# Kernel optimization log

Measured on AMD Instinct MI355X. Metric: run time of the kernel, lower is better.

Reference implementation:

```python
import jax, jax.numpy as jnp
import numpy as np

NUM_CLASSES = 10
LAMBDA_COORD = 5.0
LAMBDA_NOOBJ = 0.5
B, S, P = 2048, 26, 5 + NUM_CLASSES


def setup_inputs() -> dict:
    key = jax.random.key(0)
    k1, k2 = jax.random.split(key)
    predictions = jax.random.normal(k1, (B, S, S, P), dtype=jnp.float32)
    targets = jax.random.normal(k2, (B, S * S * P,), dtype=jnp.float32)
    return {"predictions": predictions, "targets": targets}


def reference(predictions, targets):
    b, s, _, p = predictions.shape
    pred = predictions.reshape(b, s * s, p)          # (B, S*S, 5+C)
    tgt = targets.reshape(b, s * s, -1)              # (B, S*S, 5+C)

    obj = tgt[..., 4] > 0                            # object mask per cell

    # Coordinate loss: lambda_coord * sum((pred_xywh - tgt_xywh)^2) over object cells
    coord_sq = jnp.sum((pred[..., :4] - tgt[..., :4]) ** 2, axis=-1)
    coord_loss = LAMBDA_COORD * jnp.sum(jnp.where(obj, coord_sq, 0.0))

    # Confidence loss: (sigmoid(p_conf) - t_conf)^2 on obj cells,
    # lambda_noobj * sigmoid(p_conf)^2 on no-obj cells (scalar MSE mean == squared diff)
    conf_p = jax.nn.sigmoid(pred[..., 4])
    conf_loss = jnp.sum(jnp.where(obj,
                                  (conf_p - tgt[..., 4]) ** 2,
                                  LAMBDA_NOOBJ * conf_p ** 2))

    # Classification loss: mean over C of squared diff per object cell, summed
    cls_sq = jnp.mean((pred[..., 5:5 + NUM_CLASSES] - tgt[..., 5:5 + NUM_CLASSES]) ** 2, axis=-1)
    class_loss = jnp.sum(jnp.where(obj, cls_sq, 0.0))

    total_loss = coord_loss + conf_loss + class_loss
    return (total_loss, coord_loss, conf_loss, class_loss)
```

## Files before the change

kernel.cpp:

```cpp
#include <hip/hip_runtime.h>

constexpr int   NUM_CLASSES  = 10;
constexpr float LAMBDA_COORD = 5.0f;
constexpr float LAMBDA_NOOBJ = 0.5f;
constexpr int   BLOCK = 256;
constexpr int   CELLS_PER_TILE = 256;
constexpr int   F4_PER_TILE    = 960;
constexpr int   NBLOCKS_MAX    = 2048;

__global__ __launch_bounds__(BLOCK) void yolo_main(
    const float4* __restrict__ pred4,
    const float4* __restrict__ tgt4,
    float* __restrict__ ws,
    unsigned ntiles, unsigned nblocks)
{
    __shared__ float flag[CELLS_PER_TILE + 1];

    const unsigned tid  = threadIdx.x;
    const bool     has3 = tid < (unsigned)(F4_PER_TILE - 768);

    float coord = 0.f, conf = 0.f, cls = 0.f;

    for (unsigned tile = blockIdx.x; tile < ntiles; tile += nblocks) {
        const unsigned tb = tile * F4_PER_TILE;

        float4 t[4], p[4];
        t[0] = tgt4[tb + tid];
        t[1] = tgt4[tb + tid + 256u];
        t[2] = tgt4[tb + tid + 512u];
        t[3] = has3 ? tgt4[tb + tid + 768u] : float4{0.f, 0.f, 0.f, 0.f};
        p[0] = pred4[tb + tid];
        p[1] = pred4[tb + tid + 256u];
        p[2] = pred4[tb + tid + 512u];
        p[3] = has3 ? pred4[tb + tid + 768u] : float4{0.f, 0.f, 0.f, 0.f};

        __syncthreads();

#pragma unroll
        for (int q = 0; q < 4; ++q) {
            if (q == 3 && !has3) continue;
            unsigned lb    = 4u * (tid + 256u * (unsigned)q);
            unsigned lcell = lb / 15u;
            unsigned j0    = lb - lcell * 15u;
            float tm[4] = {t[q].x, t[q].y, t[q].z, t[q].w};
#pragma unroll
            for (int m = 0; m < 4; ++m) {
                unsigned j   = j0 + (unsigned)m;
                bool     sec = j >= 15u;
                unsigned jj  = sec ? j - 15u : j;
                if (jj == 4u) flag[lcell + (sec ? 1u : 0u)] = tm[m];
            }
        }
        __syncthreads();

#pragma unroll
        for (int q = 0; q < 4; ++q) {
            if (q == 3 && !has3) continue;
            unsigned lb    = 4u * (tid + 256u * (unsigned)q);
            unsigned lcell = lb / 15u;
            unsigned j0    = lb - lcell * 15u;
            float t4a = flag[lcell];
            float t4b = flag[lcell + 1u];
            float pm[4] = {p[q].x, p[q].y, p[q].z, p[q].w};
            float tm[4] = {t[q].x, t[q].y, t[q].z, t[q].w};

            float pc = 0.f, tc = 0.f;
            bool  hasc = false;

#pragma unroll
            for (int m = 0; m < 4; ++m) {
                unsigned j   = j0 + (unsigned)m;
                bool     sec = j >= 15u;
                unsigned jj  = sec ? j - 15u : j;
                float    t4  = sec ? t4b : t4a;
                bool     obj = t4 > 0.f;

                float d  = pm[m] - tm[m];
                float sq = d * d;

                if (jj == 4u) { pc = pm[m]; tc = tm[m]; hasc = true; }
                else if (obj) {
                    if (jj < 4u) coord += sq;
                    else         cls   += sq;
                }
            }
            if (hasc) {
                float e   = __expf(-pc);
                float sig = __builtin_amdgcn_rcpf(1.f + e);
                float ds  = sig - tc;
                conf += (tc > 0.f) ? ds * ds : LAMBDA_NOOBJ * sig * sig;
            }
        }
    }

#pragma unroll
    for (int off = 32; off > 0; off >>= 1) {
        coord += __shfl_down(coord, off);
        conf  += __shfl_down(conf,  off);
        cls   += __shfl_down(cls,   off);
    }

    __shared__ float s[3][4];
    int wave = threadIdx.x >> 6, lane = threadIdx.x & 63;
    if (lane == 0) { s[0][wave] = coord; s[1][wave] = conf; s[2][wave] = cls; }
    __syncthreads();

    if (threadIdx.x == 0) {
        ws[blockIdx.x]               = s[0][0] + s[0][1] + s[0][2] + s[0][3];
        ws[nblocks + blockIdx.x]     = s[1][0] + s[1][1] + s[1][2] + s[1][3];
        ws[2 * nblocks + blockIdx.x] = s[2][0] + s[2][1] + s[2][2] + s[2][3];
    }
}

__global__ __launch_bounds__(BLOCK) void yolo_finalize(
    const float* __restrict__ ws, float* __restrict__ out, unsigned nblocks)
{
    float c0 = 0.f, c1 = 0.f, c2 = 0.f;
    for (unsigned i = threadIdx.x; i < nblocks; i += BLOCK) {
        c0 += ws[i];
        c1 += ws[nblocks + i];
        c2 += ws[2 * nblocks + i];
    }
#pragma unroll
    for (int off = 32; off > 0; off >>= 1) {
        c0 += __shfl_down(c0, off);
        c1 += __shfl_down(c1, off);
        c2 += __shfl_down(c2, off);
    }
    __shared__ float s[3][4];
    int wave = threadIdx.x >> 6, lane = threadIdx.x & 63;
    if (lane == 0) { s[0][wave] = c0; s[1][wave] = c1; s[2][wave] = c2; }
    __syncthreads();
    if (threadIdx.x == 0) {
        float coord = LAMBDA_COORD * (s[0][0] + s[0][1] + s[0][2] + s[0][3]);
        float conf  =                 s[1][0] + s[1][1] + s[1][2] + s[1][3];
        float cls   = (1.f / NUM_CLASSES) * (s[2][0] + s[2][1] + s[2][2] + s[2][3]);
        out[0] = coord + conf + cls;
        out[1] = coord;
        out[2] = conf;
        out[3] = cls;
    }
}

extern "C" void kernel_launch(void* const* d_in, const int* in_sizes, int n_in,
                              void* d_out, int out_size, void* d_ws, size_t ws_size,
                              hipStream_t stream) {
    const float* pred = (const float*)d_in[0];
    const float* tgt  = (const float*)d_in[1];
    float* out = (float*)d_out;
    float* ws  = (float*)d_ws;

    unsigned total  = (unsigned)in_sizes[0];
    unsigned ncells = total / 15u;
    unsigned ntiles = ncells / CELLS_PER_TILE;

    unsigned nblocks = NBLOCKS_MAX;
    if ((size_t)nblocks * 3 * sizeof(float) > ws_size)
        nblocks = (unsigned)(ws_size / (3 * sizeof(float)));
    if (nblocks > ntiles) nblocks = ntiles;

    yolo_main<<<nblocks, BLOCK, 0, stream>>>(
        (const float4*)pred, (const float4*)tgt, ws, ntiles, nblocks);
    yolo_finalize<<<1, BLOCK, 0, stream>>>(ws, out, nblocks);
}
```

Baseline: 184.8 us.

## Use per-wave tiles with one-shot blocks and binned atomic partial sums

Replaces the grid-stride loop over 256-cell block tiles with a one-shot grid in which each wave handles its own 64-cell tile, using a per-wave LDS flag array. This removes the block-wide barriers between the flag-write and compute phases. Per-block partials are now atomically added into 256 bins zeroed by a memset, so finalize reads a fixed number of entries. The cost is a much larger grid, an extra memset launch, atomic contention on the bins, and a change in the order of float summation.

Result: no change. 183.5 us (-0.7%).

```diff
diff --git a/kernel.cpp b/kernel.cpp
--- a/kernel.cpp
+++ b/kernel.cpp
@@ -4,92 +4,90 @@
 constexpr float LAMBDA_COORD = 5.0f;
 constexpr float LAMBDA_NOOBJ = 0.5f;
 constexpr int   BLOCK = 256;
-constexpr int   CELLS_PER_TILE = 256;
-constexpr int   F4_PER_TILE    = 960;
-constexpr int   NBLOCKS_MAX    = 2048;
+constexpr int   CELLS_PER_WAVE = 64;
+constexpr int   F4_PER_WAVE    = 240;
+constexpr int   NBINS = 256;
 
 __global__ __launch_bounds__(BLOCK) void yolo_main(
     const float4* __restrict__ pred4,
     const float4* __restrict__ tgt4,
-    float* __restrict__ ws,
-    unsigned ntiles, unsigned nblocks)
+    float* __restrict__ ws)
 {
-    __shared__ float flag[CELLS_PER_TILE + 1];
+    __shared__ float flag[4][CELLS_PER_WAVE + 1];
 
     const unsigned tid  = threadIdx.x;
-    const bool     has3 = tid < (unsigned)(F4_PER_TILE - 768);
+    const unsigned wave = tid >> 6;
+    const unsigned lane = tid & 63u;
+    const bool     has3 = lane < 48u;
+
+    const unsigned gw = blockIdx.x * 4u + wave;
+    const unsigned fb = gw * F4_PER_WAVE;
+
+    float4 t[4], p[4];
+    t[0] = tgt4[fb + lane];
+    t[1] = tgt4[fb + 64u + lane];
+    t[2] = tgt4[fb + 128u + lane];
+    t[3] = has3 ? tgt4[fb + 192u + lane] : float4{0.f, 0.f, 0.f, 0.f};
+    p[0] = pred4[fb + lane];
+    p[1] = pred4[fb + 64u + lane];
+    p[2] = pred4[fb + 128u + lane];
+    p[3] = has3 ? pred4[fb + 192u + lane] : float4{0.f, 0.f, 0.f, 0.f};
+
+#pragma unroll
+    for (int q = 0; q < 4; ++q) {
+        unsigned lf4 = (q < 3) ? (lane + 64u * (unsigned)q) : (192u + lane);
+        unsigned lb  = 4u * lf4;
+        unsigned lcell = lb / 15u;
+        unsigned j0    = lb - lcell * 15u;
+        float tm[4] = {t[q].x, t[q].y, t[q].z, t[q].w};
+#pragma unroll
+        for (int m = 0; m < 4; ++m) {
+            if (q == 3 && !has3) break;
+            unsigned j   = j0 + (unsigned)m;
+            bool     sec = j >= 15u;
+            unsigned jj  = sec ? j - 15u : j;
+            if (jj == 4u) flag[wave][lcell + (sec ? 1u : 0u)] = tm[m];
+        }
+    }
 
     float coord = 0.f, conf = 0.f, cls = 0.f;
+#pragma unroll
+    for (int q = 0; q < 4; ++q) {
+        unsigned lf4 = (q < 3) ? (lane + 64u * (unsigned)q) : (192u + lane);
+        unsigned lb  = 4u * lf4;
+        unsigned lcell = lb / 15u;
+        unsigned j0    = lb - lcell * 15u;
+        float t4a = flag[wave][lcell];
+        float t4b = flag[wave][lcell + 1u];
+        float pm[4] = {p[q].x, p[q].y, p[q].z, p[q].w};
+        float tm[4] = {t[q].x, t[q].y, t[q].z, t[q].w};
 
-    for (unsigned tile = blockIdx.x; tile < ntiles; tile += nblocks) {
-        const unsigned tb = tile * F4_PER_TILE;
-
-        float4 t[4], p[4];
-        t[0] = tgt4[tb + tid];
-        t[1] = tgt4[tb + tid + 256u];
-        t[2] = tgt4[tb + tid + 512u];
-        t[3] = has3 ? tgt4[tb + tid + 768u] : float4{0.f, 0.f, 0.f, 0.f};
-        p[0] = pred4[tb + tid];
-        p[1] = pred4[tb + tid + 256u];
-        p[2] = pred4[tb + tid + 512u];
-        p[3] = has3 ? pred4[tb + tid + 768u] : float4{0.f, 0.f, 0.f, 0.f};
-
-        __syncthreads();
+        float pc = 0.f, tc = 0.f;
+        bool  hasc = false;
 
 #pragma unroll
-        for (int q = 0; q < 4; ++q) {
-            if (q == 3 && !has3) continue;
-            unsigned lb    = 4u * (tid + 256u * (unsigned)q);
-            unsigned lcell = lb / 15u;
-            unsigned j0    = lb - lcell * 15u;
-            float tm[4] = {t[q].x, t[q].y, t[q].z, t[q].w};
-#pragma unroll
-            for (int m = 0; m < 4; ++m) {
-                unsigned j   = j0 + (unsigned)m;
-                bool     sec = j >= 15u;
-                unsigned jj  = sec ? j - 15u : j;
-                if (jj == 4u) flag[lcell + (sec ? 1u : 0u)] = tm[m];
+        for (int m = 0; m < 4; ++m) {
+            if (q == 3 && !has3) break;
+            unsigned j   = j0 + (unsigned)m;
+            bool     sec = j >= 15u;
+            unsigned jj  = sec ? j - 15u : j;
+            float    t4  = sec ? t4b : t4a;
+            bool     obj = t4 > 0.f;
+
+            float d  = pm[m] - tm[m];
+            float sq = d * d;
+
+            if (jj == 4u) { pc = pm[m]; tc = tm[m]; hasc = true; }
+            else if (obj) {
+                if (jj < 4u) coord += sq;
+                else         cls   += sq;
             }
         }
-        __syncthreads();
-
-#pragma unroll
-        for (int q = 0; q < 4; ++q) {
-            if (q == 3 && !has3) continue;
-            unsigned lb    = 4u * (tid + 256u * (unsigned)q);
-            unsigned lcell = lb / 15u;
-            unsigned j0    = lb - lcell * 15u;
-            float t4a = flag[lcell];
-            float t4b = flag[lcell + 1u];
-            float pm[4] = {p[q].x, p[q].y, p[q].z, p[q].w};
-            float tm[4] = {t[q].x, t[q].y, t[q].z, t[q].w};
-
-            float pc = 0.f, tc = 0.f;
-            bool  hasc = false;
-
-#pragma unroll
-            for (int m = 0; m < 4; ++m) {
-                unsigned j   = j0 + (unsigned)m;
-                bool     sec = j >= 15u;
-                unsigned jj  = sec ? j - 15u : j;
-                float    t4  = sec ? t4b : t4a;
-                bool     obj = t4 > 0.f;
-
-                float d  = pm[m] - tm[m];
-                float sq = d * d;
-
-                if (jj == 4u) { pc = pm[m]; tc = tm[m]; hasc = true; }
-                else if (obj) {
-                    if (jj < 4u) coord += sq;
-                    else         cls   += sq;
-                }
-            }
-            if (hasc) {
-                float e   = __expf(-pc);
-                float sig = __builtin_amdgcn_rcpf(1.f + e);
-                float ds  = sig - tc;
-                conf += (tc > 0.f) ? ds * ds : LAMBDA_NOOBJ * sig * sig;
-            }
+        if (hasc) {
+            float e   = __expf(-pc);
+            float sig = __builtin_amdgcn_rcpf(1.f + e);
+            float ds  = sig - tc;
+            conf += (tc > 0.f) ? ds * ds : LAMBDA_NOOBJ * sig * sig;
         }
     }
 
@@ -101,25 +99,25 @@
     }
 
     __shared__ float s[3][4];
-    int wave = threadIdx.x >> 6, lane = threadIdx.x & 63;
     if (lane == 0) { s[0][wave] = coord; s[1][wave] = conf; s[2][wave] = cls; }
     __syncthreads();
 
-    if (threadIdx.x == 0) {
-        ws[blockIdx.x]               = s[0][0] + s[0][1] + s[0][2] + s[0][3];
-        ws[nblocks + blockIdx.x]     = s[1][0] + s[1][1] + s[1][2] + s[1][3];
-        ws[2 * nblocks + blockIdx.x] = s[2][0] + s[2][1] + s[2][2] + s[2][3];
+    if (tid == 0) {
+        unsigned bin = (blockIdx.x & (NBINS - 1u)) * 3u;
+        atomicAdd(&ws[bin + 0], s[0][0] + s[0][1] + s[0][2] + s[0][3]);
+        atomicAdd(&ws[bin + 1], s[1][0] + s[1][1] + s[1][2] + s[1][3]);
+        atomicAdd(&ws[bin + 2], s[2][0] + s[2][1] + s[2][2] + s[2][3]);
     }
 }
 
 __global__ __launch_bounds__(BLOCK) void yolo_finalize(
-    const float* __restrict__ ws, float* __restrict__ out, unsigned nblocks)
+    const float* __restrict__ ws, float* __restrict__ out)
 {
     float c0 = 0.f, c1 = 0.f, c2 = 0.f;
-    for (unsigned i = threadIdx.x; i < nblocks; i += BLOCK) {
-        c0 += ws[i];
-        c1 += ws[nblocks + i];
-        c2 += ws[2 * nblocks + i];
+    for (unsigned i = threadIdx.x; i < (unsigned)NBINS; i += BLOCK) {
+        c0 += ws[3u * i + 0];
+        c1 += ws[3u * i + 1];
+        c2 += ws[3u * i + 2];
     }
 #pragma unroll
     for (int off = 32; off > 0; off >>= 1) {
@@ -152,14 +150,10 @@
 
     unsigned total  = (unsigned)in_sizes[0];
     unsigned ncells = total / 15u;
-    unsigned ntiles = ncells / CELLS_PER_TILE;
+    unsigned nwaves = ncells / CELLS_PER_WAVE;
+    unsigned nblk   = nwaves / 4u;
 
-    unsigned nblocks = NBLOCKS_MAX;
-    if ((size_t)nblocks * 3 * sizeof(float) > ws_size)
-        nblocks = (unsigned)(ws_size / (3 * sizeof(float)));
-    if (nblocks > ntiles) nblocks = ntiles;
-
-    yolo_main<<<nblocks, BLOCK, 0, stream>>>(
-        (const float4*)pred, (const float4*)tgt, ws, ntiles, nblocks);
-    yolo_finalize<<<1, BLOCK, 0, stream>>>(ws, out, nblocks);
+    hipMemsetAsync(ws, 0, NBINS * 3 * sizeof(float), stream);
+    yolo_main<<<nblk, BLOCK, 0, stream>>>((const float4*)pred, (const float4*)tgt, ws);
+    yolo_finalize<<<1, BLOCK, 0, stream>>>(ws, out);
 }
```
